# Optimization experiments

Hardware: AMD Instinct MI355X
Metric: run time of the kernel (lower is better)

The kernel has to match this reference:

```python
import jax, jax.numpy as jnp
import numpy as np

B, N, C = 16, 2000, 80
SCORE_THRE = 0.05
NMS_THRESH = 0.5
MAX_DET = 300
NEG = jnp.float32(-1e9)


def setup_inputs() -> dict:
    key = jax.random.key(0)
    k1, k2, k3, k4 = jax.random.split(key, 4)
    label_pre = jax.random.normal(k1, (B, N, C + 1), dtype=jnp.float32)
    bbox_pre = jax.random.normal(k2, (B, N, 4 * (C + 1)), dtype=jnp.float32)
    # valid xyxy proposal boxes in image coordinates
    xy = jax.random.uniform(k3, (B, N, 2), minval=0.0, maxval=800.0)
    wh = jax.random.uniform(k4, (B, N, 2), minval=2.0, maxval=200.0)
    proposals = jnp.concatenate([xy, xy + wh], axis=-1)
    return {"label_pre": label_pre, "bbox_pre": bbox_pre, "proposals": proposals}


def _nms(boxes, scores, iou_t):
    # Greedy NMS with fixed MAX_DET iterations; suppressed/invalid entries get score NEG.
    areas = (boxes[:, 2] - boxes[:, 0]) * (boxes[:, 3] - boxes[:, 1])

    def body(s, _):
        i = jnp.argmax(s)
        valid = s[i] > NEG * 0.5  # still a real candidate left
        b = boxes[i]
        xx1 = jnp.maximum(b[0], boxes[:, 0])
        yy1 = jnp.maximum(b[1], boxes[:, 1])
        xx2 = jnp.minimum(b[2], boxes[:, 2])
        yy2 = jnp.minimum(b[3], boxes[:, 3])
        inter = jnp.clip(xx2 - xx1, 0.0) * jnp.clip(yy2 - yy1, 0.0)
        ab = (b[2] - b[0]) * (b[3] - b[1])
        iou = inter / (ab + areas - inter + 1e-9)
        sup = (iou > iou_t) & valid
        s = jnp.where(sup, NEG, s)
        s = s.at[i].set(NEG)
        return s, (i, valid)

    _, (idx, flags) = jax.lax.scan(body, scores, None, length=MAX_DET)
    return idx, flags


def _per_image(label_logits, proposals):
    probs = jax.nn.softmax(label_logits, axis=1)          # [N, C+1]
    scores = probs[:, 1:].reshape(-1)                      # [N*C]
    labels = jnp.broadcast_to(jnp.arange(1, C + 1, dtype=jnp.int32), (N, C)).reshape(-1)
    # torch: proposal.unsqueeze(1).expand_as(bbox).reshape(-1,4); boxes = proposal (decode is dead code)
    boxes = jnp.broadcast_to(proposals[:, None, :], (N, C, 4)).reshape(-1, 4)
    area = (boxes[:, 3] - boxes[:, 1]) * (boxes[:, 2] - boxes[:, 0])
    valid = (scores > SCORE_THRE) & (area > 0.1)           # score threshold + remove_small_boxes
    s = jnp.where(valid, scores, NEG)
    # class-aware batched NMS via per-class coordinate offset (torchvision batched_nms trick)
    max_coord = jnp.max(boxes)
    boxes_off = boxes + (labels.astype(boxes.dtype) * (max_coord + 1.0))[:, None]
    idx, flags = _nms(boxes_off, s, NMS_THRESH)
    fb = flags[:, None].astype(boxes.dtype)
    out_boxes = boxes[idx] * fb                            # padded to MAX_DET, zeros where invalid
    out_labels = jnp.where(flags, labels[idx], 0)
    out_scores = jnp.where(flags, scores[idx], 0.0)
    return out_boxes, out_labels, out_scores


def reference(label_pre, bbox_pre, proposals):
    # bbox_pre is consumed by dead code in the torch source (decode result overwritten),
    # so it does not affect the output; kept as an arg for signature fidelity.
    boxes, labels, scores = jax.vmap(_per_image)(label_pre, proposals)
    return boxes, labels, scores
```

## Files before the change

### kernel.cpp

```cpp
#include <hip/hip_runtime.h>
#include <math.h>

#define NB 16
#define NN 2000
#define NC 80
#define NCL 81
#define MAXDET 300
#define NEGV (-1e9f)
#define SCORE_THRE 0.05f
#define NMS_T 0.5f
#define NBKT 4096
#define SELCAP 512
#define OVCAP 512
#define MAXM 256
#define NMS_THREADS 256

#define OFF_CTAB 0
#define OFF_OVC  81920
#define OFF_MAXC 82944
#define OFF_SCNT 83008
#define OFF_BKT  88320

__global__ void k_init_max(const float* __restrict__ prop, float* maxc) {
    int b = blockIdx.x;
    __shared__ float red[256];
    float m = -1e30f;
    const float* p = prop + (size_t)b * NN * 4;
    for (int i = threadIdx.x; i < NN * 4; i += blockDim.x) m = fmaxf(m, p[i]);
    red[threadIdx.x] = m;
    __syncthreads();
    for (int s = 128; s > 0; s >>= 1) {
        if (threadIdx.x < s) red[threadIdx.x] = fmaxf(red[threadIdx.x], red[threadIdx.x + s]);
        __syncthreads();
    }
    if (threadIdx.x == 0) maxc[b] = red[0];
}

__device__ inline void emit_cand(unsigned int* ctab, unsigned long long* bucket,
                                 unsigned int* ovcnt, unsigned long long* ov,
                                 int b, int c, unsigned int gidv, float p, int mpc) {
    unsigned int sb = __float_as_uint(p) | 0x80000000u;
    unsigned long long key = ((unsigned long long)sb << 32) |
                             (unsigned long long)(0xFFFFFFFFu - gidv);
    int pos = (int)atomicAdd(&ctab[(b * NC + c) * 16], 1u);
    if (pos < mpc) bucket[(size_t)(b * NC + c) * mpc + pos] = key;
    else { int op = (int)atomicAdd(&ovcnt[b * 16], 1u); if (op < OVCAP) ov[(size_t)b * OVCAP + op] = key; }
}

__global__ void __launch_bounds__(256) k_compact2(const float* __restrict__ logits,
                                                  const float* __restrict__ prop,
                                                  unsigned int* ctab, unsigned int* ovcnt,
                                                  unsigned long long* bucket, unsigned long long* ov,
                                                  int mpc) {
    int w = blockIdx.x * 4 + (threadIdx.x >> 6);
    int lane = threadIdx.x & 63;
    int b = w / NN, n = w % NN;

    const float* z = logits + (size_t)w * NCL;
    float z0 = z[lane];
    float z1 = (lane < NCL - 64) ? z[64 + lane] : -INFINITY;
    float m = fmaxf(z0, z1);
    for (int d = 1; d < 64; d <<= 1) m = fmaxf(m, __shfl_xor(m, d, 64));
    double e0 = exp((double)(z0 - m));
    double e1 = (lane < NCL - 64) ? exp((double)(z1 - m)) : 0.0;
    double sum = e0 + e1;
    for (int d = 1; d < 64; d <<= 1) sum += __shfl_xor(sum, d, 64);

    const float* pr = prop + (size_t)w * 4;
    float area = (pr[3] - pr[1]) * (pr[2] - pr[0]);
    bool okA = (area > 0.1f);

    if (okA && lane >= 1) {
        float p = (float)(e0 / sum);
        if (p > SCORE_THRE)
            emit_cand(ctab, bucket, ovcnt, ov, b, lane - 1, (unsigned)(n * NC + lane - 1), p, mpc);
    }
    if (okA && lane < NCL - 64) {
        float p = (float)(e1 / sum);
        if (p > SCORE_THRE)
            emit_cand(ctab, bucket, ovcnt, ov, b, 63 + lane, (unsigned)(n * NC + 63 + lane), p, mpc);
    }
}

__global__ void __launch_bounds__(NMS_THREADS) k_nms_pc(const float* __restrict__ prop,
                                                        const float* __restrict__ maxc,
                                                        const unsigned int* __restrict__ ctab,
                                                        const unsigned int* __restrict__ ovcnt,
                                                        unsigned long long* bucket,
                                                        const unsigned long long* __restrict__ ov,
                                                        unsigned int* scnt, int mpc) {
    int b = blockIdx.x / NC, cls = blockIdx.x % NC;
    int tid = threadIdx.x;
    int lane = tid & 63, wid = tid >> 6;
    unsigned long long* mybkt = bucket + (size_t)(b * NC + cls) * mpc;

    __shared__ unsigned long long keyu[MAXM];
    __shared__ unsigned long long key[MAXM];
    __shared__ float X1[MAXM], Y1[MAXM], X2[MAXM], Y2[MAXM], AR[MAXM];
    __shared__ unsigned long long msk[MAXM][4];
    __shared__ unsigned long long alive_sh[4];
    __shared__ int sh_m2, sh_base[4];

    int ct = (int)ctab[(b * NC + cls) * 16];
    int c0 = ct < mpc ? ct : mpc;
    for (int i = tid; i < c0; i += NMS_THREADS) keyu[i] = mybkt[i];
    if (tid == 0) sh_m2 = c0;
    int ovc = (int)ovcnt[b * 16]; if (ovc > OVCAP) ovc = OVCAP;
    __syncthreads();
    for (int i = tid; i < ovc; i += NMS_THREADS) {
        unsigned long long k = ov[(size_t)b * OVCAP + i];
        unsigned int gi = 0xFFFFFFFFu - (unsigned int)(k & 0xFFFFFFFFull);
        if ((int)(gi % NC) == cls) {
            int pos = atomicAdd(&sh_m2, 1);
            if (pos < MAXM) keyu[pos] = k;
        }
    }
    __syncthreads();
    int m2 = sh_m2; if (m2 > MAXM) m2 = MAXM;
    if (m2 == 0) { if (tid == 0) scnt[b * NC + cls] = 0; return; }

    if (tid < m2) {
        unsigned long long mykey = keyu[tid];
        int r = 0;
#pragma unroll 4
        for (int j = 0; j < m2; ++j) r += (keyu[j] > mykey);
        key[r] = mykey;
    }
    __syncthreads();

    float offv = (float)(cls + 1) * (maxc[b] + 1.0f);
    const float* pr = prop + (size_t)b * NN * 4;
    if (tid < m2) {
        unsigned int gi = 0xFFFFFFFFu - (unsigned int)(key[tid] & 0xFFFFFFFFull);
        int n = gi / NC;
        float4 p4 = ((const float4*)pr)[n];
        float x1 = p4.x + offv, y1 = p4.y + offv, x2 = p4.z + offv, y2 = p4.w + offv;
        X1[tid] = x1; Y1[tid] = y1; X2[tid] = x2; Y2[tid] = y2;
        AR[tid] = (x2 - x1) * (y2 - y1);
    }
    for (int i = tid; i < m2 * 4; i += NMS_THREADS) ((unsigned long long*)msk)[i] = 0ull;
    __syncthreads();

    if ((wid << 6) < m2) {
        int j = (wid << 6) + lane;
        bool jv = j < m2;
        float jx1 = 0, jy1 = 0, jx2 = 0, jy2 = 0, jar = 0;
        if (jv) { jx1 = X1[j]; jy1 = Y1[j]; jx2 = X2[j]; jy2 = Y2[j]; jar = AR[j]; }
        int imax = (wid << 6) + 64; if (imax > m2) imax = m2;
        for (int i = 0; i < imax; ++i) {
            float px1 = X1[i], py1 = Y1[i], px2 = X2[i], py2 = Y2[i], pab = AR[i];
            bool kill = false;
            if (jv && j > i) {
                float xx1 = fmaxf(px1, jx1), yy1 = fmaxf(py1, jy1);
                float xx2 = fminf(px2, jx2), yy2 = fminf(py2, jy2);
                float inter = fmaxf(xx2 - xx1, 0.0f) * fmaxf(yy2 - yy1, 0.0f);
                float iou = inter / (pab + jar - inter + 1e-9f);
                kill = iou > NMS_T;
            }
            unsigned long long km = __ballot(kill);
            if (lane == 0) msk[i][wid] = km;
        }
    }
    __syncthreads();

    if (tid == 0) {
        unsigned long long A0 = 0, A1 = 0, A2 = 0, A3 = 0;
        {
            int nn = m2;
            A0 = (nn >= 64) ? ~0ull : ((1ull << nn) - 1); nn -= 64;
            if (nn > 0) A1 = (nn >= 64) ? ~0ull : ((1ull << nn) - 1); nn -= 64;
            if (nn > 0) A2 = (nn >= 64) ? ~0ull : ((1ull << nn) - 1); nn -= 64;
            if (nn > 0) A3 = (nn >= 64) ? ~0ull : ((1ull << nn) - 1);
        }
        if (m2 <= 64) {
#pragma unroll 4
            for (int i = 0; i < m2; ++i) {
                unsigned long long row = msk[i][0];
                unsigned long long sel = 0ull - ((A0 >> i) & 1ull);
                A0 &= ~(row & sel);
            }
        } else {
            for (int i = 0; i < m2; ++i) {
                unsigned long long r0 = msk[i][0], r1 = msk[i][1],
                                   r2 = msk[i][2], r3 = msk[i][3];
                int w0 = i >> 6, bit = i & 63;
                unsigned long long cur = (w0 == 0) ? A0 : (w0 == 1) ? A1 : (w0 == 2) ? A2 : A3;
                unsigned long long sel = 0ull - ((cur >> bit) & 1ull);
                A0 &= ~(r0 & sel); A1 &= ~(r1 & sel);
                A2 &= ~(r2 & sel); A3 &= ~(r3 & sel);
            }
        }
        alive_sh[0] = A0; alive_sh[1] = A1; alive_sh[2] = A2; alive_sh[3] = A3;
        int tot = 0;
        sh_base[0] = 0;   tot += __popcll(A0);
        sh_base[1] = tot; tot += __popcll(A1);
        sh_base[2] = tot; tot += __popcll(A2);
        sh_base[3] = tot; tot += __popcll(A3);
        scnt[b * NC + cls] = (unsigned)tot;
    }
    __syncthreads();

    if (tid < m2) {
        int w = tid >> 6, bit = tid & 63;
        unsigned long long am = alive_sh[w];
        if ((am >> bit) & 1ull) {
            int pos = sh_base[w] + (int)__popcll(am & ((1ull << bit) - 1ull));
            mybkt[pos] = key[tid];
        }
    }
}

__global__ void __launch_bounds__(1024) k_merge(const float* __restrict__ prop,
                                                const unsigned int* __restrict__ scnt,
                                                const unsigned long long* __restrict__ bucket,
                                                int mpc, float* out) {
    int b = blockIdx.x;
    int tid = threadIdx.x;
    const unsigned long long* bb = bucket + (size_t)b * NC * mpc;

    __shared__ unsigned int hist[NBKT];
    __shared__ unsigned int partial[1025];
    __shared__ unsigned long long skey[SELCAP];
    __shared__ int scl[NC];
    __shared__ int Bstar, selcnt;

    for (int i = tid; i < NBKT; i += 1024) hist[i] = 0;
    for (int i = tid; i < SELCAP; i += 1024) skey[i] = 0ull;
    if (tid < NC) scl[tid] = (int)scnt[b * NC + tid];
    if (tid == 0) { Bstar = -1; selcnt = 0; }
    __syncthreads();

    int tot_slots = NC * mpc;
    for (int j = tid; j < tot_slots; j += 1024) {
        int c = j / mpc, q = j - c * mpc;
        if (q < scl[c]) {
            unsigned int sb = (unsigned int)(bb[j] >> 32);
            atomicAdd(&hist[(sb >> 15) & 0xFFFu], 1u);
        }
    }
    __syncthreads();

    unsigned int v = hist[4 * tid] + hist[4 * tid + 1] + hist[4 * tid + 2] + hist[4 * tid + 3];
    partial[tid] = v;
    if (tid == 0) partial[1024] = 0;
    __syncthreads();
    for (int off = 1; off < 1024; off <<= 1) {
        unsigned int x = (tid + off < 1024) ? partial[tid + off] : 0u;
        __syncthreads();
        partial[tid] += x;
        __syncthreads();
    }
    {
        unsigned int acc = partial[tid + 1];
        for (int q = 3; q >= 0; --q) {
            int bkt = 4 * tid + q;
            unsigned int h = hist[bkt];
            if (acc < MAXDET && acc + h >= MAXDET) Bstar = bkt;
            acc += h;
        }
    }
    __syncthreads();
    int total = (int)partial[0];
    int need = total < MAXDET ? total : MAXDET;
    int bsel = (Bstar < 0) ? 0 : Bstar;

    for (int j = tid; j < tot_slots; j += 1024) {
        int c = j / mpc, q = j - c * mpc;
        if (q < scl[c]) {
            unsigned long long k = bb[j];
            unsigned int sb = (unsigned int)(k >> 32);
            if ((int)((sb >> 15) & 0xFFFu) >= bsel) {
                int pos = atomicAdd(&selcnt, 1);
                if (pos < SELCAP) skey[pos] = k;
            }
        }
    }
    __syncthreads();

    for (int kk = 2; kk <= SELCAP; kk <<= 1) {
        for (int j = kk >> 1; j > 0; j >>= 1) {
            if (tid < SELCAP) {
                int i = tid, ixj = i ^ j;
                if (ixj > i) {
                    unsigned long long a = skey[i], c = skey[ixj];
                    bool descBlock = ((i & kk) == 0);
                    if (descBlock ? (a < c) : (a > c)) { skey[i] = c; skey[ixj] = a; }
                }
            }
            __syncthreads();
        }
    }

    const float* pr = prop + (size_t)b * NN * 4;
    float* oB = out + (size_t)b * MAXDET * 4;
    float* oL = out + (size_t)NB * MAXDET * 4 + (size_t)b * MAXDET;
    float* oS = out + (size_t)NB * MAXDET * 5 + (size_t)b * MAXDET;
    if (tid < MAXDET) {
        if (tid >= need) {
            oB[(size_t)tid * 4 + 0] = 0.0f; oB[(size_t)tid * 4 + 1] = 0.0f;
            oB[(size_t)tid * 4 + 2] = 0.0f; oB[(size_t)tid * 4 + 3] = 0.0f;
            oL[tid] = 0.0f; oS[tid] = 0.0f;
        } else {
            unsigned long long k = skey[tid];
            unsigned int sb = (unsigned int)(k >> 32);
            float sv = __uint_as_float(sb & 0x7FFFFFFFu);
            int gi = (int)(0xFFFFFFFFu - (unsigned int)(k & 0xFFFFFFFFull));
            int n = gi / NC, c = gi % NC + 1;
            oB[(size_t)tid * 4 + 0] = pr[n * 4 + 0];
            oB[(size_t)tid * 4 + 1] = pr[n * 4 + 1];
            oB[(size_t)tid * 4 + 2] = pr[n * 4 + 2];
            oB[(size_t)tid * 4 + 3] = pr[n * 4 + 3];
            oL[tid] = (float)c;
            oS[tid] = sv;
        }
    }
}

extern "C" void kernel_launch(void* const* d_in, const int* in_sizes, int n_in,
                              void* d_out, int out_size, void* d_ws, size_t ws_size,
                              hipStream_t stream) {
    const float* label_pre = (const float*)d_in[0];
    const float* proposals = (const float*)d_in[2];
    float* out = (float*)d_out;
    char* ws = (char*)d_ws;

    int mpc = 192;
    size_t ovbytes = (size_t)NB * OVCAP * 8;
    size_t need = (size_t)OFF_BKT + (size_t)NB * NC * mpc * 8 + ovbytes;
    if (ws_size < need) {
        mpc = (int)((ws_size - OFF_BKT - ovbytes) / ((size_t)NB * NC * 8));
        if (mpc < 16) mpc = 16;
    }
    if (mpc > MAXM) mpc = MAXM;

    unsigned int* ctab = (unsigned int*)(ws + OFF_CTAB);
    unsigned int* ovcnt = (unsigned int*)(ws + OFF_OVC);
    float* maxc = (float*)(ws + OFF_MAXC);
    unsigned int* scnt = (unsigned int*)(ws + OFF_SCNT);
    unsigned long long* bucket = (unsigned long long*)(ws + OFF_BKT);
    unsigned long long* ov = bucket + (size_t)NB * NC * mpc;

    hipMemsetAsync(d_ws, 0, OFF_BKT, stream);
    k_init_max<<<NB, 256, 0, stream>>>(proposals, maxc);
    k_compact2<<<NB * NN / 4, 256, 0, stream>>>(label_pre, proposals, ctab, ovcnt, bucket, ov, mpc);
    k_nms_pc<<<NB * NC, NMS_THREADS, 0, stream>>>(proposals, maxc, ctab, ovcnt, bucket, ov, scnt, mpc);
    k_merge<<<NB, 1024, 0, stream>>>(proposals, scnt, bucket, mpc, out);
}
```

Baseline: 74.63 us.

## Replace atomic candidate buckets with dense per-class slot table and fuse max

Compaction no longer appends candidates through global atomics into per-class buckets with an overflow list. It now writes every (class, proposal) score key into a dense class-major slot array, with zero marking an invalid entry. The per-image max-coordinate reduction moves into the compaction kernel, which removes the memset and one launch. The NMS kernel gathers nonzero keys per class by scanning 2000 slots. The merge kernel swaps its block scan for a wave-shuffle scan and its bitonic sort for a rank sort, trading atomic contention and extra launches for much more global write and read traffic (about 20 MB of slot writes).

```diff
diff --git a/kernel.cpp b/kernel.cpp
--- a/kernel.cpp
+++ b/kernel.cpp
@@ -6,54 +6,25 @@
 #define NC 80
 #define NCL 81
 #define MAXDET 300
-#define NEGV (-1e9f)
 #define SCORE_THRE 0.05f
 #define NMS_T 0.5f
 #define NBKT 4096
 #define SELCAP 512
-#define OVCAP 512
 #define MAXM 256
 #define NMS_THREADS 256
-
-#define OFF_CTAB 0
-#define OFF_OVC  81920
-#define OFF_MAXC 82944
-#define OFF_SCNT 83008
-#define OFF_BKT  88320
-
-__global__ void k_init_max(const float* __restrict__ prop, float* maxc) {
-    int b = blockIdx.x;
-    __shared__ float red[256];
-    float m = -1e30f;
-    const float* p = prop + (size_t)b * NN * 4;
-    for (int i = threadIdx.x; i < NN * 4; i += blockDim.x) m = fmaxf(m, p[i]);
-    red[threadIdx.x] = m;
-    __syncthreads();
-    for (int s = 128; s > 0; s >>= 1) {
-        if (threadIdx.x < s) red[threadIdx.x] = fmaxf(red[threadIdx.x], red[threadIdx.x + s]);
-        __syncthreads();
-    }
-    if (threadIdx.x == 0) maxc[b] = red[0];
-}
-
-__device__ inline void emit_cand(unsigned int* ctab, unsigned long long* bucket,
-                                 unsigned int* ovcnt, unsigned long long* ov,
-                                 int b, int c, unsigned int gidv, float p, int mpc) {
-    unsigned int sb = __float_as_uint(p) | 0x80000000u;
-    unsigned long long key = ((unsigned long long)sb << 32) |
-                             (unsigned long long)(0xFFFFFFFFu - gidv);
-    int pos = (int)atomicAdd(&ctab[(b * NC + c) * 16], 1u);
-    if (pos < mpc) bucket[(size_t)(b * NC + c) * mpc + pos] = key;
-    else { int op = (int)atomicAdd(&ovcnt[b * 16], 1u); if (op < OVCAP) ov[(size_t)b * OVCAP + op] = key; }
-}
-
-__global__ void __launch_bounds__(256) k_compact2(const float* __restrict__ logits,
-                                                  const float* __restrict__ prop,
-                                                  unsigned int* ctab, unsigned int* ovcnt,
-                                                  unsigned long long* bucket, unsigned long long* ov,
-                                                  int mpc) {
-    int w = blockIdx.x * 4 + (threadIdx.x >> 6);
-    int lane = threadIdx.x & 63;
+#define BLKS_PER_IMG (NN / 4)
+
+#define OFF_MAXC 0
+#define OFF_SCNT 256
+#define OFF_SLOT 8192
+
+__global__ void __launch_bounds__(256) k_compact(const float* __restrict__ logits,
+                                                 const float* __restrict__ prop,
+                                                 unsigned long long* __restrict__ slot,
+                                                 float* __restrict__ maxc) {
+    __shared__ float red[4];
+    int wid = threadIdx.x >> 6, lane = threadIdx.x & 63;
+    int w = blockIdx.x * 4 + wid;
     int b = w / NN, n = w % NN;
 
     const float* z = logits + (size_t)w * NCL;
@@ -70,53 +41,67 @@
     float area = (pr[3] - pr[1]) * (pr[2] - pr[0]);
     bool okA = (area > 0.1f);
 
-    if (okA && lane >= 1) {
+    unsigned long long* srow = slot + (size_t)b * NC * NN;
+    if (lane >= 1) {
+        int c = lane - 1;
         float p = (float)(e0 / sum);
-        if (p > SCORE_THRE)
-            emit_cand(ctab, bucket, ovcnt, ov, b, lane - 1, (unsigned)(n * NC + lane - 1), p, mpc);
-    }
-    if (okA && lane < NCL - 64) {
+        unsigned long long val = 0ull;
+        if (okA && p > SCORE_THRE) {
+            unsigned int gid = (unsigned)(n * NC + c);
+            unsigned int sb = __float_as_uint(p) | 0x80000000u;
+            val = ((unsigned long long)sb << 32) | (unsigned long long)(0xFFFFFFFFu - gid);
+        }
+        srow[(size_t)c * NN + n] = val;
+    }
+    if (lane < NCL - 64) {
+        int c = 63 + lane;
         float p = (float)(e1 / sum);
-        if (p > SCORE_THRE)
-            emit_cand(ctab, bucket, ovcnt, ov, b, 63 + lane, (unsigned)(n * NC + 63 + lane), p, mpc);
+        unsigned long long val = 0ull;
+        if (okA && p > SCORE_THRE) {
+            unsigned int gid = (unsigned)(n * NC + c);
+            unsigned int sb = __float_as_uint(p) | 0x80000000u;
+            val = ((unsigned long long)sb << 32) | (unsigned long long)(0xFFFFFFFFu - gid);
+        }
+        srow[(size_t)c * NN + n] = val;
+    }
+
+    if (blockIdx.x % BLKS_PER_IMG == 0) {
+        int bb = blockIdx.x / BLKS_PER_IMG;
+        const float* pp = prop + (size_t)bb * NN * 4;
+        float mm = -1e30f;
+        for (int i = threadIdx.x; i < NN * 4; i += 256) mm = fmaxf(mm, pp[i]);
+        for (int d = 1; d < 64; d <<= 1) mm = fmaxf(mm, __shfl_xor(mm, d, 64));
+        if (lane == 0) red[wid] = mm;
+        __syncthreads();
+        if (threadIdx.x == 0)
+            maxc[bb] = fmaxf(fmaxf(red[0], red[1]), fmaxf(red[2], red[3]));
     }
 }
 
-__global__ void __launch_bounds__(NMS_THREADS) k_nms_pc(const float* __restrict__ prop,
-                                                        const float* __restrict__ maxc,
-                                                        const unsigned int* __restrict__ ctab,
-                                                        const unsigned int* __restrict__ ovcnt,
-                                                        unsigned long long* bucket,
-                                                        const unsigned long long* __restrict__ ov,
-                                                        unsigned int* scnt, int mpc) {
+__global__ void __launch_bounds__(NMS_THREADS) k_nms(const float* __restrict__ prop,
+                                                     const float* __restrict__ maxc,
+                                                     unsigned long long* __restrict__ slot,
+                                                     unsigned int* __restrict__ scnt) {
     int b = blockIdx.x / NC, cls = blockIdx.x % NC;
     int tid = threadIdx.x;
     int lane = tid & 63, wid = tid >> 6;
-    unsigned long long* mybkt = bucket + (size_t)(b * NC + cls) * mpc;
+    unsigned long long* srow = slot + ((size_t)b * NC + cls) * NN;
 
     __shared__ unsigned long long keyu[MAXM];
     __shared__ unsigned long long key[MAXM];
     __shared__ float X1[MAXM], Y1[MAXM], X2[MAXM], Y2[MAXM], AR[MAXM];
     __shared__ unsigned long long msk[MAXM][4];
     __shared__ unsigned long long alive_sh[4];
-    __shared__ int sh_m2, sh_base[4];
-
-    int ct = (int)ctab[(b * NC + cls) * 16];
-    int c0 = ct < mpc ? ct : mpc;
-    for (int i = tid; i < c0; i += NMS_THREADS) keyu[i] = mybkt[i];
-    if (tid == 0) sh_m2 = c0;
-    int ovc = (int)ovcnt[b * 16]; if (ovc > OVCAP) ovc = OVCAP;
-    __syncthreads();
-    for (int i = tid; i < ovc; i += NMS_THREADS) {
-        unsigned long long k = ov[(size_t)b * OVCAP + i];
-        unsigned int gi = 0xFFFFFFFFu - (unsigned int)(k & 0xFFFFFFFFull);
-        if ((int)(gi % NC) == cls) {
-            int pos = atomicAdd(&sh_m2, 1);
-            if (pos < MAXM) keyu[pos] = k;
-        }
-    }
-    __syncthreads();
-    int m2 = sh_m2; if (m2 > MAXM) m2 = MAXM;
+    __shared__ int sh_cnt, sh_base[4];
+
+    if (tid == 0) sh_cnt = 0;
+    __syncthreads();
+    for (int n = tid; n < NN; n += NMS_THREADS) {
+        unsigned long long k = srow[n];
+        if (k) { int pos = atomicAdd(&sh_cnt, 1); if (pos < MAXM) keyu[pos] = k; }
+    }
+    __syncthreads();
+    int m2 = sh_cnt < MAXM ? sh_cnt : MAXM;
     if (m2 == 0) { if (tid == 0) scnt[b * NC + cls] = 0; return; }
 
     if (tid < m2) {
@@ -205,53 +190,54 @@
         unsigned long long am = alive_sh[w];
         if ((am >> bit) & 1ull) {
             int pos = sh_base[w] + (int)__popcll(am & ((1ull << bit) - 1ull));
-            mybkt[pos] = key[tid];
+            srow[pos] = key[tid];
         }
     }
 }
 
 __global__ void __launch_bounds__(1024) k_merge(const float* __restrict__ prop,
                                                 const unsigned int* __restrict__ scnt,
-                                                const unsigned long long* __restrict__ bucket,
-                                                int mpc, float* out) {
+                                                const unsigned long long* __restrict__ slot,
+                                                float* __restrict__ out) {
     int b = blockIdx.x;
     int tid = threadIdx.x;
-    const unsigned long long* bb = bucket + (size_t)b * NC * mpc;
+    int lane = tid & 63, wv = tid >> 6;
+    const unsigned long long* sb_ = slot + (size_t)b * NC * NN;
 
     __shared__ unsigned int hist[NBKT];
-    __shared__ unsigned int partial[1025];
     __shared__ unsigned long long skey[SELCAP];
+    __shared__ unsigned long long sorted[SELCAP];
     __shared__ int scl[NC];
+    __shared__ unsigned int wtotu[16];
     __shared__ int Bstar, selcnt;
 
     for (int i = tid; i < NBKT; i += 1024) hist[i] = 0;
-    for (int i = tid; i < SELCAP; i += 1024) skey[i] = 0ull;
     if (tid < NC) scl[tid] = (int)scnt[b * NC + tid];
     if (tid == 0) { Bstar = -1; selcnt = 0; }
     __syncthreads();
 
-    int tot_slots = NC * mpc;
-    for (int j = tid; j < tot_slots; j += 1024) {
-        int c = j / mpc, q = j - c * mpc;
+    for (int j = tid; j < NC * MAXM; j += 1024) {
+        int c = j >> 8, q = j & 255;
         if (q < scl[c]) {
-            unsigned int sb = (unsigned int)(bb[j] >> 32);
-            atomicAdd(&hist[(sb >> 15) & 0xFFFu], 1u);
-        }
-    }
-    __syncthreads();
-
-    unsigned int v = hist[4 * tid] + hist[4 * tid + 1] + hist[4 * tid + 2] + hist[4 * tid + 3];
-    partial[tid] = v;
-    if (tid == 0) partial[1024] = 0;
-    __syncthreads();
-    for (int off = 1; off < 1024; off <<= 1) {
-        unsigned int x = (tid + off < 1024) ? partial[tid + off] : 0u;
-        __syncthreads();
-        partial[tid] += x;
-        __syncthreads();
-    }
+            unsigned int s = (unsigned int)(sb_[(size_t)c * NN + q] >> 32);
+            atomicAdd(&hist[(s >> 15) & 0xFFFu], 1u);
+        }
+    }
+    __syncthreads();
+
+    unsigned int v4 = hist[4 * tid] + hist[4 * tid + 1] + hist[4 * tid + 2] + hist[4 * tid + 3];
+    unsigned int s = v4;
+    for (int d = 1; d < 64; d <<= 1) {
+        unsigned int t = __shfl_down(s, d, 64);
+        if (lane + d < 64) s += t;
+    }
+    if (lane == 0) wtotu[wv] = s;
+    __syncthreads();
+    unsigned int add = 0, tot = 0;
+    for (int u = 0; u < 16; ++u) { unsigned int x = wtotu[u]; tot += x; if (u > wv) add += x; }
+    unsigned int S_t = s + add;
     {
-        unsigned int acc = partial[tid + 1];
+        unsigned int acc = S_t - v4;
         for (int q = 3; q >= 0; --q) {
             int bkt = 4 * tid + q;
             unsigned int h = hist[bkt];
@@ -260,16 +246,15 @@
         }
     }
     __syncthreads();
-    int total = (int)partial[0];
+    int total = (int)tot;
     int need = total < MAXDET ? total : MAXDET;
     int bsel = (Bstar < 0) ? 0 : Bstar;
 
-    for (int j = tid; j < tot_slots; j += 1024) {
-        int c = j / mpc, q = j - c * mpc;
+    for (int j = tid; j < NC * MAXM; j += 1024) {
+        int c = j >> 8, q = j & 255;
         if (q < scl[c]) {
-            unsigned long long k = bb[j];
-            unsigned int sb = (unsigned int)(k >> 32);
-            if ((int)((sb >> 15) & 0xFFFu) >= bsel) {
+            unsigned long long k = sb_[(size_t)c * NN + q];
+            if ((int)(((unsigned int)(k >> 32) >> 15) & 0xFFFu) >= bsel) {
                 int pos = atomicAdd(&selcnt, 1);
                 if (pos < SELCAP) skey[pos] = k;
             }
@@ -277,19 +262,14 @@
     }
     __syncthreads();
 
-    for (int kk = 2; kk <= SELCAP; kk <<= 1) {
-        for (int j = kk >> 1; j > 0; j >>= 1) {
-            if (tid < SELCAP) {
-                int i = tid, ixj = i ^ j;
-                if (ixj > i) {
-                    unsigned long long a = skey[i], c = skey[ixj];
-                    bool descBlock = ((i & kk) == 0);
-                    if (descBlock ? (a < c) : (a > c)) { skey[i] = c; skey[ixj] = a; }
-                }
-            }
-            __syncthreads();
-        }
-    }
+    int sn = selcnt < SELCAP ? selcnt : SELCAP;
+    if (tid < sn) {
+        unsigned long long mk = skey[tid];
+        int r = 0;
+        for (int j = 0; j < sn; ++j) r += (skey[j] > mk);
+        sorted[r] = mk;
+    }
+    __syncthreads();
 
     const float* pr = prop + (size_t)b * NN * 4;
     float* oB = out + (size_t)b * MAXDET * 4;
@@ -301,7 +281,7 @@
             oB[(size_t)tid * 4 + 2] = 0.0f; oB[(size_t)tid * 4 + 3] = 0.0f;
             oL[tid] = 0.0f; oS[tid] = 0.0f;
         } else {
-            unsigned long long k = skey[tid];
+            unsigned long long k = sorted[tid];
             unsigned int sb = (unsigned int)(k >> 32);
             float sv = __uint_as_float(sb & 0x7FFFFFFFu);
             int gi = (int)(0xFFFFFFFFu - (unsigned int)(k & 0xFFFFFFFFull));
@@ -324,25 +304,11 @@
     float* out = (float*)d_out;
     char* ws = (char*)d_ws;
 
-    int mpc = 192;
-    size_t ovbytes = (size_t)NB * OVCAP * 8;
-    size_t need = (size_t)OFF_BKT + (size_t)NB * NC * mpc * 8 + ovbytes;
-    if (ws_size < need) {
-        mpc = (int)((ws_size - OFF_BKT - ovbytes) / ((size_t)NB * NC * 8));
-        if (mpc < 16) mpc = 16;
-    }
-    if (mpc > MAXM) mpc = MAXM;
-
-    unsigned int* ctab = (unsigned int*)(ws + OFF_CTAB);
-    unsigned int* ovcnt = (unsigned int*)(ws + OFF_OVC);
     float* maxc = (float*)(ws + OFF_MAXC);
     unsigned int* scnt = (unsigned int*)(ws + OFF_SCNT);
-    unsigned long long* bucket = (unsigned long long*)(ws + OFF_BKT);
-    unsigned long long* ov = bucket + (size_t)NB * NC * mpc;
-
-    hipMemsetAsync(d_ws, 0, OFF_BKT, stream);
-    k_init_max<<<NB, 256, 0, stream>>>(proposals, maxc);
-    k_compact2<<<NB * NN / 4, 256, 0, stream>>>(label_pre, proposals, ctab, ovcnt, bucket, ov, mpc);
-    k_nms_pc<<<NB * NC, NMS_THREADS, 0, stream>>>(proposals, maxc, ctab, ovcnt, bucket, ov, scnt, mpc);
-    k_merge<<<NB, 1024, 0, stream>>>(proposals, scnt, bucket, mpc, out);
+    unsigned long long* slot = (unsigned long long*)(ws + OFF_SLOT);
+
+    k_compact<<<NB * NN / 4, 256, 0, stream>>>(label_pre, proposals, slot, maxc);
+    k_nms<<<NB * NC, NMS_THREADS, 0, stream>>>(proposals, maxc, slot, scnt);
+    k_merge<<<NB, 1024, 0, stream>>>(proposals, scnt, slot, out);
 }
```

Result: no change. 76.09 us, median of 2 (+2.0%).
